# Performance work log

Measured on AMD Instinct MI355X. Metric: run time of the kernel, lower is better.

Reference implementation:

```python
import jax, jax.numpy as jnp
import numpy as np

B, H, W, CIN = 4, 32, 32, 3
COUT, NPAR = 4, 16

# Ansatz3x3 gate list: (control, target, base param index); each entry applies
# CRZ(theta[k], control, target) then CRX(theta[k+1], control, target).
GATES = [(1, 0, 0), (3, 2, 2), (2, 0, 4), (8, 7, 6),
         (5, 4, 8), (7, 6, 10), (6, 4, 12), (4, 0, 14)]
NQ = 9


def setup_inputs() -> dict:
    key = jax.random.key(0)
    k1, k2 = jax.random.split(key)
    x = jax.random.uniform(k1, (B, H, W, CIN), dtype=jnp.float32)
    q_params = jax.random.uniform(k2, (COUT, NPAR), minval=-np.pi, maxval=np.pi,
                                  dtype=jnp.float32)
    return {"x": x, "q_params": q_params}


def _rz_mat(th):
    # RZ(th) = diag(e^{-i th/2}, e^{+i th/2}); th: [C] -> [C,2,2]
    e = jnp.exp(-0.5j * th.astype(jnp.complex64))
    z = jnp.zeros_like(e)
    return jnp.stack([jnp.stack([e, z], -1), jnp.stack([z, jnp.conj(e)], -1)], -2)


def _rx_mat(th):
    # RX(th) = [[cos, -i sin], [-i sin, cos]] with half-angle; th: [C] -> [C,2,2]
    c = jnp.cos(0.5 * th).astype(jnp.complex64)
    s = (-1j * jnp.sin(0.5 * th)).astype(jnp.complex64)
    return jnp.stack([jnp.stack([c, s], -1), jnp.stack([s, c], -1)], -2)


def _apply_ctrl(state, U, control, target):
    # state: [C, P] + [2]*NQ (axis 2+q is qubit q); U: [C,2,2] applied on target
    # when control qubit is 1.
    ax_c, ax_t = 2 + control, 2 + target
    s0, s1 = jnp.split(state, 2, axis=ax_c)
    s1 = jnp.moveaxis(s1, ax_t, -1)
    s1 = jnp.einsum('cab,c...b->c...a', U, s1)
    s1 = jnp.moveaxis(s1, -1, ax_t)
    return jnp.concatenate([s0, s1], axis=ax_c)


def _quanv_forward(x, q_params):
    cout = q_params.shape[0]
    b, h, w = x.shape[0], x.shape[1], x.shape[2]
    fx, fy = h - 2, w - 2  # stride 1
    avg = jnp.mean(x, axis=-1)  # [B,H,W]
    # 3x3 patches, row-major flatten matching .flatten(): [B,fx,fy,9]
    patches = jnp.stack([avg[:, i:i + fx, j:j + fy]
                         for i in range(3) for j in range(3)], axis=-1)
    angles = 2.0 * jnp.pi * patches - jnp.pi
    # RX(angle)|0> = [cos(a/2), -i sin(a/2)] per qubit -> product state
    a0 = jnp.cos(0.5 * angles).astype(jnp.complex64)
    a1 = (-1j * jnp.sin(0.5 * angles)).astype(jnp.complex64)
    amps = jnp.stack([a0, a1], axis=-1).reshape(b * fx * fy, NQ, 2)  # [P,9,2]
    P = b * fx * fy
    state = amps[:, 0, :]  # [P,2]
    for q in range(1, NQ):
        state = state[..., None] * amps[:, q, :].reshape((P,) + (1,) * q + (2,))
    # replicate over output channels (params differ per channel)
    state = jnp.broadcast_to(state[None], (cout,) + state.shape) + 0j  # [C,P,2,...,2]
    for (ctrl, tgt, k) in GATES:
        state = _apply_ctrl(state, _rz_mat(q_params[:, k]), ctrl, tgt)
        state = _apply_ctrl(state, _rx_mat(q_params[:, k + 1]), ctrl, tgt)
    # avgZ = (p0 - p1 + 1)/2 = P(qubit0 = 0); qubit 0 is axis 2
    s = state[:, :, 0]  # [C,P] + [2]*8
    p0 = jnp.sum(s.real ** 2 + s.imag ** 2, axis=tuple(range(2, 2 + NQ - 1)))  # [C,P]
    out = jnp.zeros((b, h, w, cout), jnp.float32)
    vals = p0.reshape(cout, b, fx, fy).transpose(1, 2, 3, 0).astype(jnp.float32)
    return out.at[:, 1:1 + fx, 1:1 + fy, :].set(vals)


def reference(x, q_params):
    return _quanv_forward(x, q_params)
```

## Files before the change

### kernel.cpp

```cpp
#include <hip/hip_runtime.h>
#include <math.h>


namespace {
constexpr int kB = 4, kH = 32, kW = 32, kCIN = 3, kCOUT = 4;
constexpr int kFX = 30, kFY = 30;
constexpr float kPI = 3.14159265358979323846f;
}

#define CRZ_LL(CMASK, TMASK, K) do {                                          \
    const float cz = gc[K], sz = gs[K];                                       \
    const bool ctl = (lane & (CMASK)) != 0;                                   \
    const float ce = ctl ? cz : 1.0f;                                         \
    const float se = ctl ? (((lane & (TMASK)) != 0) ? sz : -sz) : 0.0f;       \
    _Pragma("unroll")                                                         \
    for (int r = 0; r < 8; ++r) {                                             \
        const float nre = ce * re[r] - se * im[r];                            \
        const float nim = ce * im[r] + se * re[r];                            \
        re[r] = nre; im[r] = nim;                                             \
    }                                                                         \
} while (0)

#define CRX_LL(CMASK, TMASK, K) do {                                          \
    const float cx = gc[K], sx = gs[K];                                       \
    const bool ctl = (lane & (CMASK)) != 0;                                   \
    _Pragma("unroll")                                                         \
    for (int r = 0; r < 8; ++r) {                                             \
        const float pre = __shfl_xor(re[r], (TMASK), 64);                     \
        const float pim = __shfl_xor(im[r], (TMASK), 64);                     \
        const float nre = cx * re[r] + sx * pim;                              \
        const float nim = cx * im[r] - sx * pre;                              \
        re[r] = ctl ? nre : re[r];                                            \
        im[r] = ctl ? nim : im[r];                                            \
    }                                                                         \
} while (0)

__global__ __launch_bounds__(256) void quanv9q_kernel(
    const float* __restrict__ x, const float* __restrict__ qp,
    float* __restrict__ out)
{
    const int lane = threadIdx.x & 63;
    const int wave = (blockIdx.x * blockDim.x + threadIdx.x) >> 6;
    if (wave >= kB * kFX * kFY * kCOUT) return;

    const int co  = wave & 3;
    const int p   = wave >> 2;
    const int b   = p / (kFX * kFY);
    const int rem = p - b * (kFX * kFY);
    const int pi  = rem / kFY;
    const int pj  = rem - pi * kFY;

    float myc = 0.f, mys = 0.f, mgc = 1.f, mgs = 0.f;
    if (lane < 9) {
        const int di = lane / 3, dj = lane % 3;
        const float* px = x + (((b * kH + (pi + di)) * kW + (pj + dj)) * kCIN);
        const float v = (px[0] + px[1] + px[2]) * (1.0f / 3.0f);
        const float half = kPI * v - 0.5f * kPI;
        myc = cosf(half); mys = sinf(half);
    }
    if (lane < 16) {
        const float th = 0.5f * qp[co * 16 + lane];
        mgc = cosf(th); mgs = sinf(th);
    }
    float cq[9], sq[9];
    #pragma unroll
    for (int q = 0; q < 9; ++q) { cq[q] = __shfl(myc, q, 64); sq[q] = __shfl(mys, q, 64); }
    float gc[16], gs[16];
    #pragma unroll
    for (int k = 0; k < 16; ++k) { gc[k] = __shfl(mgc, k, 64); gs[k] = __shfl(mgs, k, 64); }

    float plane_m = 1.0f;
    #pragma unroll
    for (int q = 0; q < 6; ++q)
        plane_m *= ((lane >> (5 - q)) & 1) ? sq[q] : cq[q];
    const int pcl = __popc(lane);

    float re[8], im[8];
    #pragma unroll
    for (int r = 0; r < 8; ++r) {
        const int b6 = (r >> 2) & 1, b7 = (r >> 1) & 1, b8 = r & 1;
        float m = plane_m;
        m *= b6 ? sq[6] : cq[6];
        m *= b7 ? sq[7] : cq[7];
        m *= b8 ? sq[8] : cq[8];
        const int pc = (pcl + b6 + b7 + b8) & 3;
        re[r] = (pc == 0) ? m : ((pc == 2) ? -m : 0.0f);
        im[r] = (pc == 1) ? -m : ((pc == 3) ? m : 0.0f);
    }

    CRZ_LL(16, 32, 0);  CRX_LL(16, 32, 1);
    CRZ_LL(4, 8, 2);    CRX_LL(4, 8, 3);
    CRZ_LL(8, 32, 4);   CRX_LL(8, 32, 5);

    {
        const float cz = gc[6], sz = gs[6];
        #pragma unroll
        for (int r = 1; r < 8; r += 2) {
            const float se = (r & 2) ? sz : -sz;
            const float nre = cz * re[r] - se * im[r];
            const float nim = cz * im[r] + se * re[r];
            re[r] = nre; im[r] = nim;
        }
        const float cx = gc[7], sx = gs[7];
        #pragma unroll
        for (int base = 0; base < 8; base += 4) {
            const int a = base + 1, c2 = base + 3;
            const float are = re[a], aim = im[a], bre = re[c2], bim = im[c2];
            re[a]  = cx * are + sx * bim;  im[a]  = cx * aim - sx * bre;
            re[c2] = cx * bre + sx * aim;  im[c2] = cx * bim - sx * are;
        }
    }

    CRZ_LL(1, 2, 8);    CRX_LL(1, 2, 9);

    {
        const float cz = gc[10], sz = gs[10];
        #pragma unroll
        for (int r = 0; r < 8; ++r) if (r & 2) {
            const float se = (r & 4) ? sz : -sz;
            const float nre = cz * re[r] - se * im[r];
            const float nim = cz * im[r] + se * re[r];
            re[r] = nre; im[r] = nim;
        }
        const float cx = gc[11], sx = gs[11];
        #pragma unroll
        for (int a0 = 2; a0 <= 3; ++a0) {
            const int a = a0, c2 = a0 + 4;
            const float are = re[a], aim = im[a], bre = re[c2], bim = im[c2];
            re[a]  = cx * are + sx * bim;  im[a]  = cx * aim - sx * bre;
            re[c2] = cx * bre + sx * aim;  im[c2] = cx * bim - sx * are;
        }
    }

    {
        const float cz = gc[12], sz = gs[12];
        const float se = ((lane & 2) != 0) ? sz : -sz;
        #pragma unroll
        for (int r = 4; r < 8; ++r) {
            const float nre = cz * re[r] - se * im[r];
            const float nim = cz * im[r] + se * re[r];
            re[r] = nre; im[r] = nim;
        }
        const float cx = gc[13], sx = gs[13];
        #pragma unroll
        for (int r = 4; r < 8; ++r) {
            const float pre = __shfl_xor(re[r], 2, 64);
            const float pim = __shfl_xor(im[r], 2, 64);
            const float nre = cx * re[r] + sx * pim;
            const float nim = cx * im[r] - sx * pre;
            re[r] = nre; im[r] = nim;
        }
    }

    CRZ_LL(2, 32, 14);  CRX_LL(2, 32, 15);

    float ssum = 0.0f;
    if ((lane & 32) == 0) {
        #pragma unroll
        for (int r = 0; r < 8; ++r) ssum += re[r] * re[r] + im[r] * im[r];
    }
    #pragma unroll
    for (int off = 32; off > 0; off >>= 1) ssum += __shfl_xor(ssum, off, 64);

    if (lane == 0)
        out[((b * kH + (pi + 1)) * kW + (pj + 1)) * kCOUT + co] = ssum;
}

extern "C" void kernel_launch(void* const* d_in, const int* in_sizes, int n_in,
                              void* d_out, int out_size, void* d_ws, size_t ws_size,
                              hipStream_t stream) {
    const float* x  = (const float*)d_in[0];
    const float* qp = (const float*)d_in[1];
    float* out = (float*)d_out;

    hipMemsetAsync(d_out, 0, (size_t)out_size * sizeof(float), stream);

    const int total_waves = kB * kFX * kFY * kCOUT;
    const int threads = 256;
    const int blocks = (total_waves * 64 + threads - 1) / threads;
    quanv9q_kernel<<<blocks, threads, 0, stream>>>(x, qp, out);
}
```

Before: 79.52 us.

## Remap qubits to register/lane bits and use DPP for lane swaps

Reassigns which qubits live in register index bits versus lane bits, so most controlled gates become register-local or lane-control-only and need no cross-lane shuffles. The two remaining lane-target CRX gates use DPP quad permutes instead of ds_bpermute shuffles. The initial state is rewritten with a phase change that keeps it real (imaginary part zero), and the final reduction sums half the registers with no lane predicate. Gate parameters are broadcast via readlane and sincosf replaces separate sin/cos; the bounds check and launch rounding are dropped because the wave count divides evenly.

```diff
diff --git a/kernel.cpp b/kernel.cpp
--- a/kernel.cpp
+++ b/kernel.cpp
@@ -8,31 +8,88 @@
 constexpr float kPI = 3.14159265358979323846f;
 }
 
-#define CRZ_LL(CMASK, TMASK, K) do {                                          \
-    const float cz = gc[K], sz = gs[K];                                       \
-    const bool ctl = (lane & (CMASK)) != 0;                                   \
-    const float ce = ctl ? cz : 1.0f;                                         \
-    const float se = ctl ? (((lane & (TMASK)) != 0) ? sz : -sz) : 0.0f;       \
-    _Pragma("unroll")                                                         \
-    for (int r = 0; r < 8; ++r) {                                             \
-        const float nre = ce * re[r] - se * im[r];                            \
-        const float nim = ce * im[r] + se * re[r];                            \
-        re[r] = nre; im[r] = nim;                                             \
-    }                                                                         \
+template <int CTRL>
+__device__ __forceinline__ float dpp_perm(float v) {
+    return __int_as_float(
+        __builtin_amdgcn_mov_dpp(__float_as_int(v), CTRL, 0xF, 0xF, true));
+}
+__device__ __forceinline__ float rdlane(float v, int l) {
+    return __int_as_float(__builtin_amdgcn_readlane(__float_as_int(v), l));
+}
+
+#define CRZ_LR(CB, TBIT, K) do {                                           \
+    const bool ctl = (lane & (CB)) != 0;                                   \
+    const float ce = ctl ? gc[K] : 1.0f;                                   \
+    const float se = ctl ? gs[K] : 0.0f;                                   \
+    _Pragma("unroll")                                                      \
+    for (int r = 0; r < 8; ++r) {                                          \
+        const float sg = (r & (TBIT)) ? -se : se;                          \
+        const float nr = ce * re[r] + sg * im[r];                          \
+        const float ni = ce * im[r] - sg * re[r];                          \
+        re[r] = nr; im[r] = ni;                                            \
+    }                                                                      \
 } while (0)
 
-#define CRX_LL(CMASK, TMASK, K) do {                                          \
-    const float cx = gc[K], sx = gs[K];                                       \
-    const bool ctl = (lane & (CMASK)) != 0;                                   \
-    _Pragma("unroll")                                                         \
-    for (int r = 0; r < 8; ++r) {                                             \
-        const float pre = __shfl_xor(re[r], (TMASK), 64);                     \
-        const float pim = __shfl_xor(im[r], (TMASK), 64);                     \
-        const float nre = cx * re[r] + sx * pim;                              \
-        const float nim = cx * im[r] - sx * pre;                              \
-        re[r] = ctl ? nre : re[r];                                            \
-        im[r] = ctl ? nim : im[r];                                            \
-    }                                                                         \
+#define CRX_LR(CB, TBIT, K) do {                                           \
+    const bool ctl = (lane & (CB)) != 0;                                   \
+    const float ce = ctl ? gc[K] : 1.0f;                                   \
+    const float se = ctl ? gs[K] : 0.0f;                                   \
+    _Pragma("unroll")                                                      \
+    for (int r = 0; r < 8; ++r) if (!(r & (TBIT))) {                       \
+        const int r2 = r | (TBIT);                                         \
+        const float ar = re[r], ai = im[r], br = re[r2], bi = im[r2];      \
+        re[r]  = ce * ar - se * br;  im[r]  = ce * ai - se * bi;           \
+        re[r2] = se * ar + ce * br;  im[r2] = se * ai + ce * bi;           \
+    }                                                                      \
+} while (0)
+
+#define CRZ_RR(CBIT, TBIT, K) do {                                         \
+    const float ce = gc[K], se = gs[K];                                    \
+    _Pragma("unroll")                                                      \
+    for (int r = 0; r < 8; ++r) if (r & (CBIT)) {                          \
+        const float sg = (r & (TBIT)) ? -se : se;                          \
+        const float nr = ce * re[r] + sg * im[r];                          \
+        const float ni = ce * im[r] - sg * re[r];                          \
+        re[r] = nr; im[r] = ni;                                            \
+    }                                                                      \
+} while (0)
+
+#define CRX_RR(CBIT, TBIT, K) do {                                         \
+    const float ce = gc[K], se = gs[K];                                    \
+    _Pragma("unroll")                                                      \
+    for (int r = 0; r < 8; ++r) if ((r & (CBIT)) && !(r & (TBIT))) {       \
+        const int r2 = r | (TBIT);                                         \
+        const float ar = re[r], ai = im[r], br = re[r2], bi = im[r2];      \
+        re[r]  = ce * ar - se * br;  im[r]  = ce * ai - se * bi;           \
+        re[r2] = se * ar + ce * br;  im[r2] = se * ai + ce * bi;           \
+    }                                                                      \
+} while (0)
+
+#define CRZ_LL(CB, TB, K) do {                                             \
+    const bool ctl = (lane & (CB)) != 0;                                   \
+    const float ce  = ctl ? gc[K] : 1.0f;                                  \
+    const float se0 = ctl ? gs[K] : 0.0f;                                  \
+    const float se  = (lane & (TB)) ? -se0 : se0;                          \
+    _Pragma("unroll")                                                      \
+    for (int r = 0; r < 8; ++r) {                                          \
+        const float nr = ce * re[r] + se * im[r];                          \
+        const float ni = ce * im[r] - se * re[r];                          \
+        re[r] = nr; im[r] = ni;                                            \
+    }                                                                      \
+} while (0)
+
+#define CRX_LL_DPP(CB, TB, DPPC, K) do {                                   \
+    const bool ctl = (lane & (CB)) != 0;                                   \
+    const float ce  = ctl ? gc[K] : 1.0f;                                  \
+    const float se0 = ctl ? gs[K] : 0.0f;                                  \
+    const float se  = (lane & (TB)) ? se0 : -se0;                          \
+    _Pragma("unroll")                                                      \
+    for (int r = 0; r < 8; ++r) {                                          \
+        const float pr  = dpp_perm<DPPC>(re[r]);                           \
+        const float pim = dpp_perm<DPPC>(im[r]);                           \
+        re[r] = ce * re[r] + se * pr;                                      \
+        im[r] = ce * im[r] + se * pim;                                     \
+    }                                                                      \
 } while (0)
 
 __global__ __launch_bounds__(256) void quanv9q_kernel(
@@ -40,130 +97,70 @@
     float* __restrict__ out)
 {
     const int lane = threadIdx.x & 63;
-    const int wave = (blockIdx.x * blockDim.x + threadIdx.x) >> 6;
-    if (wave >= kB * kFX * kFY * kCOUT) return;
+    const int wave = (blockIdx.x << 2) + (threadIdx.x >> 6);
 
     const int co  = wave & 3;
     const int p   = wave >> 2;
     const int b   = p / (kFX * kFY);
     const int rem = p - b * (kFX * kFY);
-    const int pi  = rem / kFY;
-    const int pj  = rem - pi * kFY;
+    const int oy  = rem / kFY;
+    const int ox  = rem - oy * kFY;
 
-    float myc = 0.f, mys = 0.f, mgc = 1.f, mgs = 0.f;
+    float myc = 0.f, mys = 0.f, mgc = 0.f, mgs = 0.f;
     if (lane < 9) {
-        const int di = lane / 3, dj = lane % 3;
-        const float* px = x + (((b * kH + (pi + di)) * kW + (pj + dj)) * kCIN);
+        const int di = lane / 3, dj = lane - (lane / 3) * 3;
+        const float* px = x + (((b * kH + (oy + di)) * kW + (ox + dj)) * kCIN);
         const float v = (px[0] + px[1] + px[2]) * (1.0f / 3.0f);
-        const float half = kPI * v - 0.5f * kPI;
-        myc = cosf(half); mys = sinf(half);
+        sincosf(kPI * v - 0.5f * kPI, &mys, &myc);
     }
     if (lane < 16) {
-        const float th = 0.5f * qp[co * 16 + lane];
-        mgc = cosf(th); mgs = sinf(th);
+        sincosf(0.5f * qp[co * 16 + lane], &mgs, &mgc);
     }
     float cq[9], sq[9];
     #pragma unroll
     for (int q = 0; q < 9; ++q) { cq[q] = __shfl(myc, q, 64); sq[q] = __shfl(mys, q, 64); }
     float gc[16], gs[16];
     #pragma unroll
-    for (int k = 0; k < 16; ++k) { gc[k] = __shfl(mgc, k, 64); gs[k] = __shfl(mgs, k, 64); }
+    for (int k = 0; k < 16; ++k) { gc[k] = rdlane(mgc, k); gs[k] = rdlane(mgs, k); }
 
-    float plane_m = 1.0f;
-    #pragma unroll
-    for (int q = 0; q < 6; ++q)
-        plane_m *= ((lane >> (5 - q)) & 1) ? sq[q] : cq[q];
-    const int pcl = __popc(lane);
+    float pm = 1.0f;
+    pm *= (lane & 1)  ? sq[7] : cq[7];
+    pm *= (lane & 2)  ? sq[6] : cq[6];
+    pm *= (lane & 4)  ? sq[8] : cq[8];
+    pm *= (lane & 8)  ? sq[5] : cq[5];
+    pm *= (lane & 16) ? sq[3] : cq[3];
+    pm *= (lane & 32) ? sq[1] : cq[1];
 
     float re[8], im[8];
+    {
+        const float a0 = pm * cq[0], a1 = pm * sq[0];
+        const float b00 = a0 * cq[2], b01 = a0 * sq[2];
+        const float b10 = a1 * cq[2], b11 = a1 * sq[2];
+        re[0] = b00 * cq[4]; re[1] = b00 * sq[4];
+        re[2] = b01 * cq[4]; re[3] = b01 * sq[4];
+        re[4] = b10 * cq[4]; re[5] = b10 * sq[4];
+        re[6] = b11 * cq[4]; re[7] = b11 * sq[4];
+    }
     #pragma unroll
-    for (int r = 0; r < 8; ++r) {
-        const int b6 = (r >> 2) & 1, b7 = (r >> 1) & 1, b8 = r & 1;
-        float m = plane_m;
-        m *= b6 ? sq[6] : cq[6];
-        m *= b7 ? sq[7] : cq[7];
-        m *= b8 ? sq[8] : cq[8];
-        const int pc = (pcl + b6 + b7 + b8) & 3;
-        re[r] = (pc == 0) ? m : ((pc == 2) ? -m : 0.0f);
-        im[r] = (pc == 1) ? -m : ((pc == 3) ? m : 0.0f);
-    }
+    for (int r = 0; r < 8; ++r) im[r] = 0.0f;
 
-    CRZ_LL(16, 32, 0);  CRX_LL(16, 32, 1);
-    CRZ_LL(4, 8, 2);    CRX_LL(4, 8, 3);
-    CRZ_LL(8, 32, 4);   CRX_LL(8, 32, 5);
-
-    {
-        const float cz = gc[6], sz = gs[6];
-        #pragma unroll
-        for (int r = 1; r < 8; r += 2) {
-            const float se = (r & 2) ? sz : -sz;
-            const float nre = cz * re[r] - se * im[r];
-            const float nim = cz * im[r] + se * re[r];
-            re[r] = nre; im[r] = nim;
-        }
-        const float cx = gc[7], sx = gs[7];
-        #pragma unroll
-        for (int base = 0; base < 8; base += 4) {
-            const int a = base + 1, c2 = base + 3;
-            const float are = re[a], aim = im[a], bre = re[c2], bim = im[c2];
-            re[a]  = cx * are + sx * bim;  im[a]  = cx * aim - sx * bre;
-            re[c2] = cx * bre + sx * aim;  im[c2] = cx * bim - sx * are;
-        }
-    }
-
-    CRZ_LL(1, 2, 8);    CRX_LL(1, 2, 9);
-
-    {
-        const float cz = gc[10], sz = gs[10];
-        #pragma unroll
-        for (int r = 0; r < 8; ++r) if (r & 2) {
-            const float se = (r & 4) ? sz : -sz;
-            const float nre = cz * re[r] - se * im[r];
-            const float nim = cz * im[r] + se * re[r];
-            re[r] = nre; im[r] = nim;
-        }
-        const float cx = gc[11], sx = gs[11];
-        #pragma unroll
-        for (int a0 = 2; a0 <= 3; ++a0) {
-            const int a = a0, c2 = a0 + 4;
-            const float are = re[a], aim = im[a], bre = re[c2], bim = im[c2];
-            re[a]  = cx * are + sx * bim;  im[a]  = cx * aim - sx * bre;
-            re[c2] = cx * bre + sx * aim;  im[c2] = cx * bim - sx * are;
-        }
-    }
-
-    {
-        const float cz = gc[12], sz = gs[12];
-        const float se = ((lane & 2) != 0) ? sz : -sz;
-        #pragma unroll
-        for (int r = 4; r < 8; ++r) {
-            const float nre = cz * re[r] - se * im[r];
-            const float nim = cz * im[r] + se * re[r];
-            re[r] = nre; im[r] = nim;
-        }
-        const float cx = gc[13], sx = gs[13];
-        #pragma unroll
-        for (int r = 4; r < 8; ++r) {
-            const float pre = __shfl_xor(re[r], 2, 64);
-            const float pim = __shfl_xor(im[r], 2, 64);
-            const float nre = cx * re[r] + sx * pim;
-            const float nim = cx * im[r] - sx * pre;
-            re[r] = nre; im[r] = nim;
-        }
-    }
-
-    CRZ_LL(2, 32, 14);  CRX_LL(2, 32, 15);
+    CRZ_LR(32, 4, 0);   CRX_LR(32, 4, 1);
+    CRZ_LR(16, 2, 2);   CRX_LR(16, 2, 3);
+    CRZ_RR(2, 4, 4);    CRX_RR(2, 4, 5);
+    CRZ_LL(4, 1, 6);    CRX_LL_DPP(4, 1, 0xB1, 7);
+    CRZ_LR(8, 1, 8);    CRX_LR(8, 1, 9);
+    CRZ_LL(1, 2, 10);   CRX_LL_DPP(1, 2, 0x4E, 11);
+    CRZ_LR(2, 1, 12);   CRX_LR(2, 1, 13);
+    CRZ_RR(1, 4, 14);   CRX_RR(1, 4, 15);
 
     float ssum = 0.0f;
-    if ((lane & 32) == 0) {
-        #pragma unroll
-        for (int r = 0; r < 8; ++r) ssum += re[r] * re[r] + im[r] * im[r];
-    }
+    #pragma unroll
+    for (int r = 0; r < 4; ++r) ssum += re[r] * re[r] + im[r] * im[r];
     #pragma unroll
     for (int off = 32; off > 0; off >>= 1) ssum += __shfl_xor(ssum, off, 64);
 
     if (lane == 0)
-        out[((b * kH + (pi + 1)) * kW + (pj + 1)) * kCOUT + co] = ssum;
+        out[((b * kH + (oy + 1)) * kW + (ox + 1)) * kCOUT + co] = ssum;
 }
 
 extern "C" void kernel_launch(void* const* d_in, const int* in_sizes, int n_in,
@@ -177,6 +174,6 @@
 
     const int total_waves = kB * kFX * kFY * kCOUT;
     const int threads = 256;
-    const int blocks = (total_waves * 64 + threads - 1) / threads;
+    const int blocks = total_waves * 64 / threads;
     quanv9q_kernel<<<blocks, threads, 0, stream>>>(x, qp, out);
 }
```

New measurement: 73.80 us. 7.2% less time.
